# Kernel tuning notes

Hardware: AMD Instinct MI355X
Metric: run time of the kernel (lower is better)

## Reference

```python
import jax, jax.numpy as jnp
import numpy as np

N = 100000   # nodes
E = 1600000  # edges
D = 64       # hidden_channels (heads=1, concat)
NEG_SLOPE = 0.2


def setup_inputs() -> dict:
    key = jax.random.key(0)
    ks = jax.random.split(key, 16)
    s = (1.0 / np.sqrt(D)).astype(np.float32) if hasattr(np.sqrt(D), 'astype') else 1.0 / np.sqrt(D)
    s = 1.0 / float(np.sqrt(D))
    inp = {
        "x": jax.random.normal(ks[0], (N, D), jnp.float32),
        "edge_index": jax.random.randint(ks[1], (2, E), 0, N, dtype=jnp.int32).astype(jnp.int64),
        "edge_attr": jax.random.normal(ks[2], (E, 1), jnp.float32),
        # layer 1 params (PyG GATConv, heads=1): lin, lin_edge, att_src, att_dst, att_edge, bias
        "W1":  jax.random.normal(ks[3], (D, D), jnp.float32) * s,
        "We1": jax.random.normal(ks[4], (1, D), jnp.float32) * s,
        "as1": jax.random.normal(ks[5], (D,), jnp.float32) * s,
        "ad1": jax.random.normal(ks[6], (D,), jnp.float32) * s,
        "ae1": jax.random.normal(ks[7], (D,), jnp.float32) * s,
        "b1":  jnp.zeros((D,), jnp.float32),
        # layer 2 params
        "W2":  jax.random.normal(ks[8], (D, D), jnp.float32) * s,
        "We2": jax.random.normal(ks[9], (1, D), jnp.float32) * s,
        "as2": jax.random.normal(ks[10], (D,), jnp.float32) * s,
        "ad2": jax.random.normal(ks[11], (D,), jnp.float32) * s,
        "ae2": jax.random.normal(ks[12], (D,), jnp.float32) * s,
        "b2":  jnp.zeros((D,), jnp.float32),
    }
    return inp


def _gat_layer(x, src, dst, edge_attr, W, We, a_src, a_dst, a_edge, bias):
    """PyG GATConv, heads=1, add_self_loops=False, edge_dim=1."""
    n = x.shape[0]
    h = x @ W                      # [N, D]  transformed node features
    he = edge_attr @ We            # [E, D]  transformed edge features
    # per-node attention logits, gathered per edge
    alpha = ((h * a_src).sum(-1)[src]
             + (h * a_dst).sum(-1)[dst]
             + (he * a_edge).sum(-1))               # [E]
    alpha = jax.nn.leaky_relu(alpha, NEG_SLOPE)
    # segment softmax over incoming edges of each dst node
    m = jax.ops.segment_max(alpha, dst, num_segments=n)   # [N]
    m = jnp.where(jnp.isfinite(m), m, 0.0)
    e = jnp.exp(alpha - m[dst])                            # [E]
    denom = jax.ops.segment_sum(e, dst, num_segments=n) + 1e-16
    w = e / denom[dst]                                     # [E]
    # weighted scatter-add aggregation of source features
    out = jax.ops.segment_sum(h[src] * w[:, None], dst, num_segments=n)
    return out + bias


def reference(x, edge_index, edge_attr,
              W1, We1, as1, ad1, ae1, b1,
              W2, We2, as2, ad2, ae2, b2):
    src = edge_index[0]
    dst = edge_index[1]
    h = _gat_layer(x, src, dst, edge_attr, W1, We1, as1, ad1, ae1, b1)
    h = jax.nn.relu(h)
    out = _gat_layer(h, src, dst, edge_attr, W2, We2, as2, ad2, ae2, b2)
    return out
```

## Files before the change

### kernel.cpp

```cpp
#include <hip/hip_runtime.h>
#include <hip/hip_fp16.h>
#include <stdint.h>

#define D 64
constexpr float NEG_SLOPE = 0.2f;
#define NPB_SHIFT 9
#define NPB 512
#define PCHUNK 4096

__global__ void k_ce(const float* __restrict__ We1, const float* __restrict__ ae1,
                     const float* __restrict__ We2, const float* __restrict__ ae2,
                     float* __restrict__ ce){
  int lane = threadIdx.x;
  float p1 = We1[lane] * ae1[lane];
  float p2 = We2[lane] * ae2[lane];
  #pragma unroll
  for (int off = 32; off; off >>= 1){ p1 += __shfl_xor(p1, off); p2 += __shfl_xor(p2, off); }
  if (lane == 0){ ce[0] = p1; ce[1] = p2; }
}

__global__ __launch_bounds__(256) void k_gemm_dots(
    const float* __restrict__ X, const float* __restrict__ W,
    const float* __restrict__ a_s, const float* __restrict__ a_d,
    __half* __restrict__ H, float* __restrict__ asrc, float* __restrict__ adst, int n)
{
  __shared__ float sX[4 * 512];
  int lane = threadIdx.x & 63;
  int wv   = threadIdx.x >> 6;
  float* tile = sX + wv * 512;
  int wid  = blockIdx.x * 4 + wv;
  int nw   = gridDim.x * 4;
  float Wc[64];
  #pragma unroll
  for (int k = 0; k < 64; ++k) Wc[k] = W[k * D + lane];
  float asv = a_s[lane], adv = a_d[lane];
  int ngrp = (n + 7) >> 3;
  for (int g = wid; g < ngrp; g += nw){
    int r0 = g << 3;
    if (r0 + 8 <= n){
      const float4* Xg = (const float4*)(X + (size_t)r0 * D);
      float4 t0 = Xg[lane * 2], t1 = Xg[lane * 2 + 1];
      ((float4*)tile)[lane * 2]     = t0;
      ((float4*)tile)[lane * 2 + 1] = t1;
      __builtin_amdgcn_wave_barrier();
      float acc[8];
      #pragma unroll
      for (int j = 0; j < 8; ++j) acc[j] = 0.f;
      #pragma unroll
      for (int j = 0; j < 8; ++j){
        #pragma unroll
        for (int kb = 0; kb < 16; ++kb){
          float4 xv = ((const float4*)(tile + j * 64))[kb];
          acc[j] = fmaf(xv.x, Wc[kb * 4 + 0], acc[j]);
          acc[j] = fmaf(xv.y, Wc[kb * 4 + 1], acc[j]);
          acc[j] = fmaf(xv.z, Wc[kb * 4 + 2], acc[j]);
          acc[j] = fmaf(xv.w, Wc[kb * 4 + 3], acc[j]);
        }
      }
      #pragma unroll
      for (int j = 0; j < 8; ++j) H[(size_t)(r0 + j) * D + lane] = __float2half(acc[j]);
      #pragma unroll
      for (int j = 0; j < 8; ++j){
        float ps = acc[j] * asv, pd = acc[j] * adv;
        #pragma unroll
        for (int off = 32; off; off >>= 1){ ps += __shfl_xor(ps, off); pd += __shfl_xor(pd, off); }
        if (lane == 0){ asrc[r0 + j] = ps; adst[r0 + j] = pd; }
      }
    } else {
      for (int j = 0; r0 + j < n; ++j){
        float acc = 0.f;
        #pragma unroll
        for (int kb = 0; kb < 16; ++kb){
          float4 xv = *(const float4*)(X + (size_t)(r0 + j) * D + kb * 4);
          acc = fmaf(xv.x, Wc[kb * 4 + 0], acc);
          acc = fmaf(xv.y, Wc[kb * 4 + 1], acc);
          acc = fmaf(xv.z, Wc[kb * 4 + 2], acc);
          acc = fmaf(xv.w, Wc[kb * 4 + 3], acc);
        }
        H[(size_t)(r0 + j) * D + lane] = __float2half(acc);
        float ps = acc * asv, pd = acc * adv;
        #pragma unroll
        for (int off = 32; off; off >>= 1){ ps += __shfl_xor(ps, off); pd += __shfl_xor(pd, off); }
        if (lane == 0){ asrc[r0 + j] = ps; adst[r0 + j] = pd; }
      }
    }
  }
}


__global__ __launch_bounds__(256) void k_bhist(const int* __restrict__ dst,
    int* __restrict__ C, int nchunk, int e, int nbkt){
  __shared__ int hist[256];
  int tid = threadIdx.x, c = blockIdx.x;
  if (tid < nbkt) hist[tid] = 0;
  __syncthreads();
  int c0 = c * PCHUNK;
  #pragma unroll
  for (int k = 0; k < PCHUNK / 256; ++k){
    int i = c0 + tid + (k << 8);
    if (i < e) atomicAdd(&hist[dst[i] >> NPB_SHIFT], 1);
  }
  __syncthreads();
  if (tid < nbkt) C[tid * nchunk + c] = hist[tid];
}

__global__ __launch_bounds__(512) void k_cscan(int* __restrict__ C,
    int* __restrict__ btot, int nchunk){
  __shared__ int s[512];
  int b = blockIdx.x, tid = threadIdx.x;
  int v = (tid < nchunk) ? C[b * nchunk + tid] : 0;
  s[tid] = v; __syncthreads();
  #pragma unroll
  for (int off = 1; off < 512; off <<= 1){
    int t = (tid >= off) ? s[tid - off] : 0;
    __syncthreads();
    s[tid] += t;
    __syncthreads();
  }
  if (tid < nchunk) C[b * nchunk + tid] = s[tid] - v;
  if (tid == 511) btot[b] = s[511];
}

__global__ __launch_bounds__(256) void k_bscan(const int* __restrict__ btot,
    int* __restrict__ gbase, int nbkt){
  __shared__ int s[256];
  int tid = threadIdx.x;
  int v = (tid < nbkt) ? btot[tid] : 0;
  s[tid] = v; __syncthreads();
  #pragma unroll
  for (int off = 1; off < 256; off <<= 1){
    int t = (tid >= off) ? s[tid - off] : 0;
    __syncthreads();
    s[tid] += t;
    __syncthreads();
  }
  if (tid < nbkt) gbase[tid] = s[tid] - v;
  if (tid == 255) gbase[nbkt] = s[255];
}

__global__ __launch_bounds__(256) void k_part(const int* __restrict__ src,
    const int* __restrict__ dst, const float* __restrict__ ea,
    const int* __restrict__ gbase, const int* __restrict__ C, int nchunk,
    int2* __restrict__ staging, int e, int nbkt){
  __shared__ int base[256], cnt[256];
  int tid = threadIdx.x, c = blockIdx.x;
  if (tid < nbkt){ base[tid] = gbase[tid] + C[tid * nchunk + c]; cnt[tid] = 0; }
  __syncthreads();
  int c0 = c * PCHUNK;
  int w0[PCHUNK / 256], w1[PCHUNK / 256], bk[PCHUNK / 256];
  #pragma unroll
  for (int k = 0; k < PCHUNK / 256; ++k){
    int i = c0 + tid + (k << 8);
    bk[k] = -1;
    if (i < e){
      int d = dst[i];
      bk[k] = d >> NPB_SHIFT;
      w0[k] = src[i] | ((d & (NPB - 1)) << 17);
      w1[k] = __float_as_int(ea[i]);
    }
  }
  #pragma unroll
  for (int k = 0; k < PCHUNK / 256; ++k){
    if (bk[k] >= 0){
      int pos = base[bk[k]] + atomicAdd(&cnt[bk[k]], 1);
      staging[pos] = make_int2(w0[k], w1[k]);
    }
  }
}

__global__ __launch_bounds__(512) void k_bucket(const int* __restrict__ gbase,
    const int2* __restrict__ staging, int2* __restrict__ edges,
    int* __restrict__ rowptr, int n, int nbkt){
  __shared__ int degL[NPB], sc[NPB];
  int b = blockIdx.x, tid = threadIdx.x;
  int node0 = b << NPB_SHIFT;
  int nn = min(NPB, n - node0);
  int base = gbase[b], endj = gbase[b + 1];
  degL[tid] = 0;
  __syncthreads();
  for (int j = base + tid; j < endj; j += NPB)
    atomicAdd(&degL[staging[j].x >> 17], 1);
  __syncthreads();
  int dv = degL[tid];
  sc[tid] = dv;
  __syncthreads();
  #pragma unroll
  for (int off = 1; off < NPB; off <<= 1){
    int t = (tid >= off) ? sc[tid - off] : 0;
    __syncthreads();
    sc[tid] += t;
    __syncthreads();
  }
  int ex = sc[tid] - dv;
  if (tid < nn) rowptr[node0 + tid] = base + ex;
  if (b == nbkt - 1 && tid == 0) rowptr[n] = base + sc[NPB - 1];
  __syncthreads();
  degL[tid] = ex;
  __syncthreads();
  for (int j = base + tid; j < endj; j += NPB){
    int2 w = staging[j];
    int dloc = w.x >> 17;
    int pos = base + atomicAdd(&degL[dloc], 1);
    edges[pos] = make_int2(w.x & 0x1FFFF, w.y);
  }
}

__global__ __launch_bounds__(256) void k_node_fused(
    const int* __restrict__ rowptr, const int2* __restrict__ edges,
    const float* __restrict__ asrc, const float* __restrict__ adst,
    const float* __restrict__ ce, int ce_idx,
    const __half* __restrict__ H, const float* __restrict__ bias,
    float* __restrict__ out, int n, int relu)
{
  int v = blockIdx.x * 4 + (threadIdx.x >> 6);
  int lane = threadIdx.x & 63;
  if (v >= n) return;
  int start = rowptr[v], end = rowptr[v + 1];
  int deg = end - start;
  if (deg == 0){
    float bv = bias[lane];
    float r = relu ? fmaxf(bv, 0.f) : bv;
    out[(size_t)v * D + lane] = r;
    return;
  }
  float adv = adst[v];
  float cev = ce[ce_idx];
  if (deg <= 64){
    int my_s = 0; float my_e = 0.f;
    if (lane < deg){
      int2 pr = edges[start + lane];
      my_s = pr.x;
      float a = asrc[pr.x] + adv + __int_as_float(pr.y) * cev;
      a = a > 0.f ? a : NEG_SLOPE * a;
      my_e = __expf(a);
    }
    int half = lane >> 5;
    int fp   = lane & 31;
    const __half2* H2 = (const __half2*)H;
    int sP[8]; float wP[8]; __half2 uP[8];
    #pragma unroll
    for (int p = 0; p < 8; ++p) sP[p] = __shfl(my_s, 2 * p + half);
    #pragma unroll
    for (int p = 0; p < 8; ++p) uP[p] = H2[(size_t)sP[p] * 32 + fp];
    float ss = my_e;
    #pragma unroll
    for (int off = 32; off; off >>= 1) ss += __shfl_xor(ss, off);
    float inv = 1.f / (ss + 1e-16f);
    #pragma unroll
    for (int p = 0; p < 8; ++p) wP[p] = __shfl(my_e, 2 * p + half);
    float accx = 0.f, accy = 0.f;
    #pragma unroll
    for (int p = 0; p < 8; ++p){
      float2 hv = __half22float2(uP[p]);
      accx = fmaf(hv.x, wP[p], accx);
      accy = fmaf(hv.y, wP[p], accy);
    }
    for (int k = 16; k < deg; k += 16){
      #pragma unroll
      for (int p = 0; p < 8; ++p){
        int ix = k + 2 * p + half; ix = ix > 63 ? 63 : ix;
        sP[p] = __shfl(my_s, ix);
      }
      #pragma unroll
      for (int p = 0; p < 8; ++p) uP[p] = H2[(size_t)sP[p] * 32 + fp];
      #pragma unroll
      for (int p = 0; p < 8; ++p){
        int ix = k + 2 * p + half; ix = ix > 63 ? 63 : ix;
        wP[p] = __shfl(my_e, ix);
      }
      #pragma unroll
      for (int p = 0; p < 8; ++p){
        float2 hv = __half22float2(uP[p]);
        accx = fmaf(hv.x, wP[p], accx);
        accy = fmaf(hv.y, wP[p], accy);
      }
    }
    accx += __shfl_xor(accx, 32);
    accy += __shfl_xor(accy, 32);
    if (lane < 32){
      float2 bv2 = ((const float2*)bias)[fp];
      float2 r;
      r.x = accx * inv + bv2.x;
      r.y = accy * inv + bv2.y;
      if (relu){ r.x = fmaxf(r.x, 0.f); r.y = fmaxf(r.y, 0.f); }
      ((float2*)(out + (size_t)v * D))[fp] = r;
    }
  } else {
    float bv = bias[lane];
    float acc0 = 0.f, acc1 = 0.f, acc2 = 0.f, acc3 = 0.f;
    float ss = 0.f;
    for (int j0 = start; j0 < end; j0 += 64){
      int j = j0 + lane;
      int my_s = 0; float my_e = 0.f;
      if (j < end){
        int2 pr = edges[j];
        float a = asrc[pr.x] + adv + __int_as_float(pr.y) * cev;
        a = a > 0.f ? a : NEG_SLOPE * a;
        my_e = __expf(a);
        my_s = pr.x;
      }
      ss += my_e;
      int cnt = min(64, end - j0);
      int k = 0;
      for (; k + 4 <= cnt; k += 4){
        int s0 = __shfl(my_s, k+0), s1 = __shfl(my_s, k+1);
        int s2 = __shfl(my_s, k+2), s3 = __shfl(my_s, k+3);
        float w0 = __shfl(my_e, k+0), w1 = __shfl(my_e, k+1);
        float w2 = __shfl(my_e, k+2), w3 = __shfl(my_e, k+3);
        float h0 = __half2float(H[(size_t)s0 * D + lane]);
        float h1 = __half2float(H[(size_t)s1 * D + lane]);
        float h2 = __half2float(H[(size_t)s2 * D + lane]);
        float h3 = __half2float(H[(size_t)s3 * D + lane]);
        acc0 = fmaf(h0, w0, acc0); acc1 = fmaf(h1, w1, acc1);
        acc2 = fmaf(h2, w2, acc2); acc3 = fmaf(h3, w3, acc3);
      }
      for (; k < cnt; ++k){
        int s0 = __shfl(my_s, k);
        float w0 = __shfl(my_e, k);
        acc0 = fmaf(__half2float(H[(size_t)s0 * D + lane]), w0, acc0);
      }
    }
    #pragma unroll
    for (int off = 32; off; off >>= 1) ss += __shfl_xor(ss, off);
    float inv = 1.f / (ss + 1e-16f);
    float acc = (acc0 + acc1) + (acc2 + acc3);
    float r = acc * inv + bv;
    if (relu) r = fmaxf(r, 0.f);
    out[(size_t)v * D + lane] = r;
  }
}

extern "C" void kernel_launch(void* const* d_in, const int* in_sizes, int n_in,
                              void* d_out, int out_size, void* d_ws, size_t ws_size,
                              hipStream_t stream)
{
  const float* x    = (const float*)d_in[0];
  const int*   ei   = (const int*)d_in[1];
  const float* ea   = (const float*)d_in[2];
  const float* W1   = (const float*)d_in[3];
  const float* We1  = (const float*)d_in[4];
  const float* as1  = (const float*)d_in[5];
  const float* ad1  = (const float*)d_in[6];
  const float* ae1  = (const float*)d_in[7];
  const float* b1   = (const float*)d_in[8];
  const float* W2   = (const float*)d_in[9];
  const float* We2  = (const float*)d_in[10];
  const float* as2  = (const float*)d_in[11];
  const float* ad2  = (const float*)d_in[12];
  const float* ae2  = (const float*)d_in[13];
  const float* b2   = (const float*)d_in[14];
  float* out = (float*)d_out;

  int n = in_sizes[0] / D;
  int e = in_sizes[1] / 2;
  const int* srcp = ei;
  const int* dstp = ei + e;

  int nbkt   = (n + NPB - 1) / NPB;
  int nchunk = (e + PCHUNK - 1) / PCHUNK;

  char* p = (char*)d_ws;
  __half* buf_h  = (__half*)p; p += (size_t)n * D * 2;
  float* buf_x2  = (float*)p;  p += (size_t)n * D * 4;
  float* asrc    = (float*)p;  p += (size_t)n * 4;
  float* adst    = (float*)p;  p += (size_t)n * 4;
  int*   rowptr  = (int*)p;    p += (size_t)(n + 16) * 4;
  int*   gbase   = (int*)p;    p += (size_t)(nbkt + 4) * 4;
  int*   btot    = (int*)p;    p += (size_t)(nbkt + 4) * 4;
  int*   C       = (int*)p;    p += (size_t)nbkt * nchunk * 4;
  float* ce      = (float*)p;  p += 64;
  int2*  edges   = (int2*)p;   p += (size_t)e * 8;
  int2*  staging = (int2*)buf_x2;

  int gR = (n + 3) / 4;
  int gG = ((n + 7) / 8 + 3) / 4;

  k_ce<<<1, 64, 0, stream>>>(We1, ae1, We2, ae2, ce);
  k_bhist<<<nchunk, 256, 0, stream>>>(dstp, C, nchunk, e, nbkt);
  k_cscan<<<nbkt, 512, 0, stream>>>(C, btot, nchunk);
  k_bscan<<<1, 256, 0, stream>>>(btot, gbase, nbkt);
  k_part<<<nchunk, 256, 0, stream>>>(srcp, dstp, ea, gbase, C, nchunk, staging, e, nbkt);
  k_bucket<<<nbkt, NPB, 0, stream>>>(gbase, staging, edges, rowptr, n, nbkt);

  k_gemm_dots<<<gG, 256, 0, stream>>>(x, W1, as1, ad1, buf_h, asrc, adst, n);
  k_node_fused<<<gR, 256, 0, stream>>>(rowptr, edges, asrc, adst, ce, 0, buf_h, b1, buf_x2, n, 1);

  k_gemm_dots<<<gG, 256, 0, stream>>>(buf_x2, W2, as2, ad2, buf_h, asrc, adst, n);
  k_node_fused<<<gR, 256, 0, stream>>>(rowptr, edges, asrc, adst, ce, 1, buf_h, b2, out, n, 0);
}
```

Baseline: 298.2 us.

## Process two nodes per wavefront in node aggregation with 8-byte gathers

```diff
diff --git a/kernel.cpp b/kernel.cpp
--- a/kernel.cpp
+++ b/kernel.cpp
@@ -212,121 +212,187 @@
     const __half* __restrict__ H, const float* __restrict__ bias,
     float* __restrict__ out, int n, int relu)
 {
-  int v = blockIdx.x * 4 + (threadIdx.x >> 6);
   int lane = threadIdx.x & 63;
-  if (v >= n) return;
-  int start = rowptr[v], end = rowptr[v + 1];
+  int wv   = threadIdx.x >> 6;
+  int vbase = (blockIdx.x * 4 + wv) * 2;
+  if (vbase >= n) return;
+  int h  = lane >> 5;
+  int li = lane & 31;
+  int v  = vbase + h;
+  bool vok = v < n;
+  int start = 0, end = 0;
+  if (vok){ start = rowptr[v]; end = rowptr[v + 1]; }
   int deg = end - start;
-  if (deg == 0){
-    float bv = bias[lane];
-    float r = relu ? fmaxf(bv, 0.f) : bv;
-    out[(size_t)v * D + lane] = r;
-    return;
-  }
-  float adv = adst[v];
+  int degmax = max(deg, __shfl_xor(deg, 32));
   float cev = ce[ce_idx];
-  if (deg <= 64){
+
+  if (degmax <= 32){
     int my_s = 0; float my_e = 0.f;
-    if (lane < deg){
-      int2 pr = edges[start + lane];
+    if (li < deg){
+      int2 pr = edges[start + li];
       my_s = pr.x;
-      float a = asrc[pr.x] + adv + __int_as_float(pr.y) * cev;
+      float a = asrc[pr.x] + adst[v] + __int_as_float(pr.y) * cev;
       a = a > 0.f ? a : NEG_SLOPE * a;
       my_e = __expf(a);
     }
-    int half = lane >> 5;
-    int fp   = lane & 31;
-    const __half2* H2 = (const __half2*)H;
-    int sP[8]; float wP[8]; __half2 uP[8];
+    int sub = li >> 4;
+    int fq  = li & 15;
+    const uint2* H2 = (const uint2*)H;
+    int eb = h * 32 + sub;
+    int sP[8]; float wP[8]; uint2 uP[8];
     #pragma unroll
-    for (int p = 0; p < 8; ++p) sP[p] = __shfl(my_s, 2 * p + half);
+    for (int p = 0; p < 8; ++p) sP[p] = __shfl(my_s, eb + 2 * p);
     #pragma unroll
-    for (int p = 0; p < 8; ++p) uP[p] = H2[(size_t)sP[p] * 32 + fp];
+    for (int p = 0; p < 8; ++p) uP[p] = H2[(size_t)sP[p] * 16 + fq];
     float ss = my_e;
     #pragma unroll
-    for (int off = 32; off; off >>= 1) ss += __shfl_xor(ss, off);
+    for (int off = 16; off; off >>= 1) ss += __shfl_xor(ss, off);
     float inv = 1.f / (ss + 1e-16f);
     #pragma unroll
-    for (int p = 0; p < 8; ++p) wP[p] = __shfl(my_e, 2 * p + half);
-    float accx = 0.f, accy = 0.f;
+    for (int p = 0; p < 8; ++p) wP[p] = __shfl(my_e, eb + 2 * p);
+    float a0 = 0.f, a1 = 0.f, a2 = 0.f, a3 = 0.f;
     #pragma unroll
     for (int p = 0; p < 8; ++p){
-      float2 hv = __half22float2(uP[p]);
-      accx = fmaf(hv.x, wP[p], accx);
-      accy = fmaf(hv.y, wP[p], accy);
-    }
-    for (int k = 16; k < deg; k += 16){
+      __half2 q0 = *(const __half2*)&uP[p].x;
+      __half2 q1 = *(const __half2*)&uP[p].y;
+      float2 f0 = __half22float2(q0);
+      float2 f1 = __half22float2(q1);
+      a0 = fmaf(f0.x, wP[p], a0);
+      a1 = fmaf(f0.y, wP[p], a1);
+      a2 = fmaf(f1.x, wP[p], a2);
+      a3 = fmaf(f1.y, wP[p], a3);
+    }
+    if (degmax > 16){
+      #pragma unroll
+      for (int p = 0; p < 8; ++p) sP[p] = __shfl(my_s, eb + 16 + 2 * p);
+      #pragma unroll
+      for (int p = 0; p < 8; ++p) uP[p] = H2[(size_t)sP[p] * 16 + fq];
+      #pragma unroll
+      for (int p = 0; p < 8; ++p) wP[p] = __shfl(my_e, eb + 16 + 2 * p);
       #pragma unroll
       for (int p = 0; p < 8; ++p){
-        int ix = k + 2 * p + half; ix = ix > 63 ? 63 : ix;
-        sP[p] = __shfl(my_s, ix);
-      }
-      #pragma unroll
-      for (int p = 0; p < 8; ++p) uP[p] = H2[(size_t)sP[p] * 32 + fp];
-      #pragma unroll
-      for (int p = 0; p < 8; ++p){
-        int ix = k + 2 * p + half; ix = ix > 63 ? 63 : ix;
-        wP[p] = __shfl(my_e, ix);
-      }
-      #pragma unroll
-      for (int p = 0; p < 8; ++p){
-        float2 hv = __half22float2(uP[p]);
-        accx = fmaf(hv.x, wP[p], accx);
-        accy = fmaf(hv.y, wP[p], accy);
-      }
-    }
-    accx += __shfl_xor(accx, 32);
-    accy += __shfl_xor(accy, 32);
-    if (lane < 32){
-      float2 bv2 = ((const float2*)bias)[fp];
-      float2 r;
-      r.x = accx * inv + bv2.x;
-      r.y = accy * inv + bv2.y;
-      if (relu){ r.x = fmaxf(r.x, 0.f); r.y = fmaxf(r.y, 0.f); }
-      ((float2*)(out + (size_t)v * D))[fp] = r;
+        __half2 q0 = *(const __half2*)&uP[p].x;
+        __half2 q1 = *(const __half2*)&uP[p].y;
+        float2 f0 = __half22float2(q0);
+        float2 f1 = __half22float2(q1);
+        a0 = fmaf(f0.x, wP[p], a0);
+        a1 = fmaf(f0.y, wP[p], a1);
+        a2 = fmaf(f1.x, wP[p], a2);
+        a3 = fmaf(f1.y, wP[p], a3);
+      }
+    }
+    a0 += __shfl_xor(a0, 16);
+    a1 += __shfl_xor(a1, 16);
+    a2 += __shfl_xor(a2, 16);
+    a3 += __shfl_xor(a3, 16);
+    if (vok && li < 16){
+      float4 bv = ((const float4*)bias)[li];
+      float4 r;
+      r.x = a0 * inv + bv.x;
+      r.y = a1 * inv + bv.y;
+      r.z = a2 * inv + bv.z;
+      r.w = a3 * inv + bv.w;
+      if (relu){
+        r.x = fmaxf(r.x, 0.f); r.y = fmaxf(r.y, 0.f);
+        r.z = fmaxf(r.z, 0.f); r.w = fmaxf(r.w, 0.f);
+      }
+      ((float4*)(out + (size_t)v * D))[li] = r;
     }
   } else {
-    float bv = bias[lane];
-    float acc0 = 0.f, acc1 = 0.f, acc2 = 0.f, acc3 = 0.f;
-    float ss = 0.f;
-    for (int j0 = start; j0 < end; j0 += 64){
-      int j = j0 + lane;
-      int my_s = 0; float my_e = 0.f;
-      if (j < end){
-        int2 pr = edges[j];
-        float a = asrc[pr.x] + adv + __int_as_float(pr.y) * cev;
-        a = a > 0.f ? a : NEG_SLOPE * a;
-        my_e = __expf(a);
-        my_s = pr.x;
-      }
-      ss += my_e;
-      int cnt = min(64, end - j0);
-      int k = 0;
-      for (; k + 4 <= cnt; k += 4){
-        int s0 = __shfl(my_s, k+0), s1 = __shfl(my_s, k+1);
-        int s2 = __shfl(my_s, k+2), s3 = __shfl(my_s, k+3);
-        float w0 = __shfl(my_e, k+0), w1 = __shfl(my_e, k+1);
-        float w2 = __shfl(my_e, k+2), w3 = __shfl(my_e, k+3);
-        float h0 = __half2float(H[(size_t)s0 * D + lane]);
-        float h1 = __half2float(H[(size_t)s1 * D + lane]);
-        float h2 = __half2float(H[(size_t)s2 * D + lane]);
-        float h3 = __half2float(H[(size_t)s3 * D + lane]);
-        acc0 = fmaf(h0, w0, acc0); acc1 = fmaf(h1, w1, acc1);
-        acc2 = fmaf(h2, w2, acc2); acc3 = fmaf(h3, w3, acc3);
-      }
-      for (; k < cnt; ++k){
-        int s0 = __shfl(my_s, k);
-        float w0 = __shfl(my_e, k);
-        acc0 = fmaf(__half2float(H[(size_t)s0 * D + lane]), w0, acc0);
-      }
-    }
-    #pragma unroll
-    for (int off = 32; off; off >>= 1) ss += __shfl_xor(ss, off);
-    float inv = 1.f / (ss + 1e-16f);
-    float acc = (acc0 + acc1) + (acc2 + acc3);
-    float r = acc * inv + bv;
-    if (relu) r = fmaxf(r, 0.f);
-    out[(size_t)v * D + lane] = r;
+    for (int t = 0; t < 2; ++t){
+      int vv = vbase + t;
+      if (vv >= n) break;
+      int st = rowptr[vv], en = rowptr[vv + 1];
+      int dg = en - st;
+      if (dg == 0){
+        float bv = bias[lane];
+        float r = relu ? fmaxf(bv, 0.f) : bv;
+        out[(size_t)vv * D + lane] = r;
+        continue;
+      }
+      float adv = adst[vv];
+      if (dg <= 64){
+        int my_s = 0; float my_e = 0.f;
+        if (lane < dg){
+          int2 pr = edges[st + lane];
+          my_s = pr.x;
+          float a = asrc[pr.x] + adv + __int_as_float(pr.y) * cev;
+          a = a > 0.f ? a : NEG_SLOPE * a;
+          my_e = __expf(a);
+        }
+        int hf = lane >> 5;
+        int fp = lane & 31;
+        const __half2* Hp = (const __half2*)H;
+        float ss = my_e;
+        #pragma unroll
+        for (int off = 32; off; off >>= 1) ss += __shfl_xor(ss, off);
+        float inv = 1.f / (ss + 1e-16f);
+        float accx = 0.f, accy = 0.f;
+        for (int k = 0; k < dg; k += 16){
+          #pragma unroll
+          for (int p = 0; p < 8; ++p){
+            int ix = k + 2 * p + hf; ix = ix > 63 ? 63 : ix;
+            int s0 = __shfl(my_s, ix);
+            float w0 = __shfl(my_e, ix);
+            float2 hv = __half22float2(Hp[(size_t)s0 * 32 + fp]);
+            accx = fmaf(hv.x, w0, accx);
+            accy = fmaf(hv.y, w0, accy);
+          }
+        }
+        accx += __shfl_xor(accx, 32);
+        accy += __shfl_xor(accy, 32);
+        if (lane < 32){
+          float2 bv2 = ((const float2*)bias)[fp];
+          float2 r;
+          r.x = accx * inv + bv2.x;
+          r.y = accy * inv + bv2.y;
+          if (relu){ r.x = fmaxf(r.x, 0.f); r.y = fmaxf(r.y, 0.f); }
+          ((float2*)(out + (size_t)vv * D))[fp] = r;
+        }
+      } else {
+        float bv = bias[lane];
+        float c0 = 0.f, c1 = 0.f, c2 = 0.f, c3 = 0.f;
+        float ss = 0.f;
+        for (int j0 = st; j0 < en; j0 += 64){
+          int j = j0 + lane;
+          int my_s = 0; float my_e = 0.f;
+          if (j < en){
+            int2 pr = edges[j];
+            float a = asrc[pr.x] + adv + __int_as_float(pr.y) * cev;
+            a = a > 0.f ? a : NEG_SLOPE * a;
+            my_e = __expf(a);
+            my_s = pr.x;
+          }
+          ss += my_e;
+          int cnt = min(64, en - j0);
+          int k = 0;
+          for (; k + 4 <= cnt; k += 4){
+            int s0 = __shfl(my_s, k+0), s1 = __shfl(my_s, k+1);
+            int s2 = __shfl(my_s, k+2), s3 = __shfl(my_s, k+3);
+            float w0 = __shfl(my_e, k+0), w1 = __shfl(my_e, k+1);
+            float w2 = __shfl(my_e, k+2), w3 = __shfl(my_e, k+3);
+            float h0 = __half2float(H[(size_t)s0 * D + lane]);
+            float h1 = __half2float(H[(size_t)s1 * D + lane]);
+            float h2 = __half2float(H[(size_t)s2 * D + lane]);
+            float h3 = __half2float(H[(size_t)s3 * D + lane]);
+            c0 = fmaf(h0, w0, c0); c1 = fmaf(h1, w1, c1);
+            c2 = fmaf(h2, w2, c2); c3 = fmaf(h3, w3, c3);
+          }
+          for (; k < cnt; ++k){
+            int s0 = __shfl(my_s, k);
+            float w0 = __shfl(my_e, k);
+            c0 = fmaf(__half2float(H[(size_t)s0 * D + lane]), w0, c0);
+          }
+        }
+        #pragma unroll
+        for (int off = 32; off; off >>= 1) ss += __shfl_xor(ss, off);
+        float inv = 1.f / (ss + 1e-16f);
+        float acc = (c0 + c1) + (c2 + c3);
+        float r = acc * inv + bv;
+        if (relu) r = fmaxf(r, 0.f);
+        out[(size_t)vv * D + lane] = r;
+      }
+    }
   }
 }
 
@@ -372,7 +438,8 @@
   int2*  edges   = (int2*)p;   p += (size_t)e * 8;
   int2*  staging = (int2*)buf_x2;
 
-  int gR = (n + 3) / 4;
+  int pairs = (n + 1) / 2;
+  int gR = (pairs + 3) / 4;
   int gG = ((n + 7) / 8 + 3) / 4;
 
   k_ce<<<1, 64, 0, stream>>>(We1, ae1, We2, ae2, ce);
```

Result: faster. 281.5 us (-5.6%).
